# Optimization experiments

Hardware: AMD Instinct MI355X
Metric: run time of the kernel (lower is better)

## Reference

```python
import jax, jax.numpy as jnp
import numpy as np

N = 50000      # nodes
E = 800000     # edges (avg degree 16)
D_IN = 128
D_H = 128
D_OUT = 64
SLOPE = 0.2    # leaky-relu negative slope (from the 0.2 constants in the graph)


def setup_inputs() -> dict:
    key = jax.random.key(0)
    ks = jax.random.split(key, 18)
    def w(k, shape, fan_in):
        return jax.random.normal(k, shape, jnp.float32) / np.sqrt(fan_in)
    inp = {
        "x": jax.random.normal(ks[0], (N, D_IN), jnp.float32),
        "W0": w(ks[1], (D_IN, D_H), D_IN),
        "b0": jnp.zeros((D_H,), jnp.float32),
        "Wq1": w(ks[2], (D_H, D_H), D_H),
        "bq1": jnp.zeros((D_H,), jnp.float32),
        "Wp1": w(ks[3], (D_H, D_H), D_H),
        "bp1": jnp.zeros((D_H,), jnp.float32),
        "a1": 0.1 * w(ks[4], (D_H,), D_H),
        "bg2": jnp.zeros((D_H,), jnp.float32),
        "Wq2": w(ks[5], (D_H, D_OUT), D_H),
        "bq2": jnp.zeros((D_OUT,), jnp.float32),
        "Wp2": w(ks[6], (D_H, D_OUT), D_H),
        "bp2": jnp.zeros((D_OUT,), jnp.float32),
        "a2": 0.1 * w(ks[7], (D_OUT,), D_OUT),
        "b_out": jnp.zeros((D_OUT,), jnp.float32),
        "src": jax.random.randint(ks[8], (E,), 0, N),
        "dst": jax.random.randint(ks[9], (E,), 0, N),
        "num_nodes": N,
    }
    return inp


def _gat_block(m, src, dst, Wq, bq, Wp, bp, a, n):
    # m: [N, d_in]; q/p: [N, d]
    q = m @ Wq + bq
    p = m @ Wp + bp
    # edge scores: s_e = sum_d leaky_relu(q[dst_e] + p[src_e]) * a_d   [E]
    e = jax.nn.leaky_relu(q[dst] + p[src], SLOPE)          # [E, d]
    s = jnp.einsum("ed,d->e", e, a)                        # [E]
    es = jnp.exp(s)                                        # unstabilized exp, as in source graph
    denom = jax.ops.segment_sum(es, dst, num_segments=n)   # [N]
    alpha = es / denom[dst]                                # [E] edge softmax over incoming edges
    # aggregate messages alpha_e * p[src_e] into dst nodes
    agg = jax.ops.segment_sum(alpha[:, None] * p[src], dst, num_segments=n)  # [N, d]
    return agg


def reference(x, W0, b0, Wq1, bq1, Wp1, bp1, a1, bg2, Wq2, bq2, Wp2, bp2, a2, b_out, src, dst, num_nodes):
    m1 = jax.nn.gelu(x @ W0 + b0, approximate=False)       # erf GELU per graph constants
    h1 = _gat_block(m1, src, dst, Wq1, bq1, Wp1, bp1, a1, num_nodes)
    m2 = jax.nn.gelu(h1 + bg2, approximate=False)
    h2 = _gat_block(m2, src, dst, Wq2, bq2, Wp2, bp2, a2, num_nodes)
    return h2 + b_out
```

## Files before the change

### kernel.cpp

```cpp
#include <hip/hip_runtime.h>
#include <hip/hip_bf16.h>
#include <math.h>


#define SLOPE 0.2f

typedef __attribute__((ext_vector_type(8))) __bf16 bf16x8;
typedef __attribute__((ext_vector_type(4))) float f32x4;

__device__ __forceinline__ float gelu_erf(float x) {
    return 0.5f * x * (1.0f + erff(x * 0.70710678118654752f));
}

__device__ __forceinline__ unsigned short f2bf(float f) {
    unsigned int u = __float_as_uint(f);
    return (unsigned short)((u + 0x7fffu + ((u >> 16) & 1u)) >> 16);
}
__device__ __forceinline__ float bf2f(unsigned short h) {
    return __uint_as_float((unsigned int)h << 16);
}

__device__ __forceinline__ float row16_sum(float x) {
    x += __int_as_float(__builtin_amdgcn_update_dpp(0, __float_as_int(x), 0x121, 0xF, 0xF, true));
    x += __int_as_float(__builtin_amdgcn_update_dpp(0, __float_as_int(x), 0x122, 0xF, 0xF, true));
    x += __int_as_float(__builtin_amdgcn_update_dpp(0, __float_as_int(x), 0x124, 0xF, 0xF, true));
    x += __int_as_float(__builtin_amdgcn_update_dpp(0, __float_as_int(x), 0x128, 0xF, 0xF, true));
    return x;
}

__device__ __forceinline__ int swz(int off) { return off ^ ((off >> 4) & 0x70); }

__global__ __launch_bounds__(256) void pack_w(
    const float* __restrict__ W0,  const float* __restrict__ Wq1,
    const float* __restrict__ Wp1, const float* __restrict__ Wq2,
    const float* __restrict__ Wp2,
    unsigned short* __restrict__ P0,  unsigned short* __restrict__ Pq1,
    unsigned short* __restrict__ Pp1, unsigned short* __restrict__ Pq2,
    unsigned short* __restrict__ Pp2)
{
    const float* W; unsigned short* P; int C;
    switch (blockIdx.y) {
        case 0:  W = W0;  P = P0;  C = 128; break;
        case 1:  W = Wq1; P = Pq1; C = 128; break;
        case 2:  W = Wp1; P = Pp1; C = 128; break;
        case 3:  W = Wq2; P = Pq2; C = 64;  break;
        default: W = Wp2; P = Pp2; C = 64;  break;
    }
    int i = blockIdx.x * 256 + threadIdx.x;
    int CE = C * 128;
    if (i >= CE) return;
    int j = i & 7, l = (i >> 3) & 63, ks = (i >> 9) & 3, ct = i >> 11;
    int k = ks * 32 + ((l >> 4) << 3) + j;
    int n = ct * 16 + (l & 15);
    float v = W[k * C + n];
    unsigned short hb = f2bf(v);
    P[i] = hb;
    P[CE + i] = f2bf(v - bf2f(hb));
}

template <int C, bool TWO, int EPI>
__global__ __launch_bounds__(256) void mfma_gemm(
    const float* __restrict__ Af,
    const unsigned short* __restrict__ AHg, const unsigned short* __restrict__ ALg,
    const unsigned short* __restrict__ P1, const float* __restrict__ b1,
    const unsigned short* __restrict__ P2, const float* __restrict__ b2,
    float* __restrict__ outq, unsigned short* __restrict__ outp,
    unsigned short* __restrict__ o1hi, unsigned short* __restrict__ o1lo,
    int N)
{
    constexpr int CE  = C * 128;
    constexpr int CTT = (TWO ? 2 : 1) * (C / 16);
    constexpr int CTW = CTT / 4;
    constexpr int QCT = C / 16;

    __shared__ __align__(16) unsigned char lds[32768];

    const int t = threadIdx.x;
    const int lane = t & 63;
    const int w = t >> 6;
    const int row0 = blockIdx.x * 64;
    const int mcol = lane & 15;
    const int hk = lane >> 4;

    if constexpr (EPI == 0) {
#pragma unroll
        for (int i = 0; i < 8; i++) {
            int idx = t + i * 256;
            int row = idx >> 5;
            int gr = row0 + row;
            float4 v = make_float4(0.f, 0.f, 0.f, 0.f);
            if (gr < N) v = *reinterpret_cast<const float4*>(Af + (size_t)gr * 128 + (idx & 31) * 4);
            const float* f = reinterpret_cast<const float*>(&v);
            unsigned int h[4], l[4];
#pragma unroll
            for (int j = 0; j < 4; j++) {
                unsigned short hb = f2bf(f[j]);
                h[j] = hb;
                l[j] = f2bf(f[j] - bf2f(hb));
            }
            int so = swz(row * 256 + (idx & 31) * 8);
            *reinterpret_cast<uint2*>(&lds[so])         = make_uint2(h[0] | (h[1] << 16), h[2] | (h[3] << 16));
            *reinterpret_cast<uint2*>(&lds[16384 + so]) = make_uint2(l[0] | (l[1] << 16), l[2] | (l[3] << 16));
        }
    } else {
#pragma unroll
        for (int i = 0; i < 4; i++) {
            int idx = t + i * 256;
            int row = idx >> 4;
            int gr = row0 + row;
            uint4 vh = make_uint4(0, 0, 0, 0), vl = make_uint4(0, 0, 0, 0);
            if (gr < N) {
                vh = *reinterpret_cast<const uint4*>(AHg + (size_t)gr * 128 + (idx & 15) * 8);
                vl = *reinterpret_cast<const uint4*>(ALg + (size_t)gr * 128 + (idx & 15) * 8);
            }
            int so = swz(row * 256 + (idx & 15) * 16);
            *reinterpret_cast<uint4*>(&lds[so])         = vh;
            *reinterpret_cast<uint4*>(&lds[16384 + so]) = vl;
        }
    }
    __syncthreads();

    f32x4 acc[CTW][4];
#pragma unroll
    for (int c = 0; c < CTW; c++)
#pragma unroll
        for (int rf = 0; rf < 4; rf++) acc[c][rf] = (f32x4){0.f, 0.f, 0.f, 0.f};

#pragma unroll
    for (int ks = 0; ks < 4; ks++) {
        bf16x8 ah[4], al[4];
#pragma unroll
        for (int rf = 0; rf < 4; rf++) {
            int so = swz((rf * 16 + mcol) * 256 + ks * 64 + hk * 16);
            ah[rf] = *reinterpret_cast<const bf16x8*>(&lds[so]);
            al[rf] = *reinterpret_cast<const bf16x8*>(&lds[16384 + so]);
        }
#pragma unroll
        for (int c = 0; c < CTW; c++) {
            int ctg = w * CTW + c;
            bool isq = (!TWO) || (ctg < QCT);
            int ct = isq ? ctg : ctg - QCT;
            const unsigned short* P = isq ? P1 : P2;
            const unsigned short* Wp = P + ((ct * 4 + ks) * 64 + lane) * 8;
            bf16x8 bh = *reinterpret_cast<const bf16x8*>(Wp);
            bf16x8 bl = *reinterpret_cast<const bf16x8*>(Wp + CE);
#pragma unroll
            for (int rf = 0; rf < 4; rf++) {
                acc[c][rf] = __builtin_amdgcn_mfma_f32_16x16x32_bf16(ah[rf], bh, acc[c][rf], 0, 0, 0);
                acc[c][rf] = __builtin_amdgcn_mfma_f32_16x16x32_bf16(al[rf], bh, acc[c][rf], 0, 0, 0);
                acc[c][rf] = __builtin_amdgcn_mfma_f32_16x16x32_bf16(ah[rf], bl, acc[c][rf], 0, 0, 0);
            }
        }
    }

    __syncthreads();

    if constexpr (EPI == 0) {
#pragma unroll
        for (int c = 0; c < CTW; c++) {
            int col = (w * CTW + c) * 16 + mcol;
            float bv = b1[col];
#pragma unroll
            for (int rf = 0; rf < 4; rf++) {
#pragma unroll
                for (int r = 0; r < 4; r++) {
                    int row = rf * 16 + hk * 4 + r;
                    float v = gelu_erf(acc[c][rf][r] + bv);
                    unsigned short hb = f2bf(v);
                    int bo = row * 256 + col * 2;
                    *reinterpret_cast<unsigned short*>(&lds[swz(bo)])         = hb;
                    *reinterpret_cast<unsigned short*>(&lds[16384 + swz(bo)]) = f2bf(v - bf2f(hb));
                }
            }
        }
        __syncthreads();
#pragma unroll
        for (int i = 0; i < 8; i++) {
            int idx = t + i * 256;
            int pl = idx >> 10;
            int j = idx & 1023;
            int row = j >> 4;
            int gr = row0 + row;
            if (gr < N) {
                uint4 v = *reinterpret_cast<const uint4*>(&lds[pl * 16384 + swz(row * 256 + (j & 15) * 16)]);
                unsigned short* dp = pl ? o1lo : o1hi;
                *reinterpret_cast<uint4*>(dp + (size_t)gr * 128 + (j & 15) * 8) = v;
            }
        }
    } else {
#pragma unroll
        for (int c = 0; c < CTW; c++) {
            int ctg = w * CTW + c;
            bool isq = ctg < QCT;
            int ct = isq ? ctg : ctg - QCT;
            int col = ct * 16 + mcol;
            float bv = (isq ? b1 : b2)[col];
#pragma unroll
            for (int rf = 0; rf < 4; rf++) {
#pragma unroll
                for (int r = 0; r < 4; r++) {
                    int row = rf * 16 + hk * 4 + r;
                    int gr = row0 + row;
                    float v = acc[c][rf][r] + bv;
                    if (isq) {
                        if (gr < N) outq[(size_t)gr * C + col] = v;
                    } else {
                        *reinterpret_cast<unsigned short*>(&lds[swz(row * 256 + col * 2)]) = f2bf(v);
                    }
                }
            }
        }
        __syncthreads();
        constexpr int SLOTS = C / 8;
#pragma unroll
        for (int i = 0; i < (64 * SLOTS) / 256; i++) {
            int idx = t + i * 256;
            int row = idx / SLOTS;
            int sl = idx % SLOTS;
            int gr = row0 + row;
            if (gr < N)
                *reinterpret_cast<uint4*>(outp + (size_t)gr * C + sl * 8) =
                    *reinterpret_cast<const uint4*>(&lds[swz(row * 256 + sl * 16)]);
        }
    }
}


__global__ __launch_bounds__(256) void hist_coarse(
    const int* __restrict__ dst, int* __restrict__ gh, int E, int CB)
{
    __shared__ int cnt[4096];
    const int blk = blockIdx.x;
    const int t = threadIdx.x;
    for (int b = t; b < CB; b += 256) cnt[b] = 0;
    __syncthreads();
    const int epb = (E + 63) / 64;
    const int s = blk * epb;
    const int e_ = (s + epb < E) ? s + epb : E;
    for (int i = s + t; i < e_; i += 256)
        atomicAdd(&cnt[dst[i] >> 4], 1);
    __syncthreads();
    for (int b = t; b < CB; b += 256)
        gh[b * 64 + blk] = cnt[b];
}

__global__ __launch_bounds__(256) void scan1_kernel(const int* __restrict__ gh,
                                                    int* __restrict__ gscan,
                                                    int* __restrict__ bsum, int M)
{
    __shared__ int lds[256];
    int t = threadIdx.x;
    int i = blockIdx.x * 256 + t;
    int v = (i < M) ? gh[i] : 0;
    lds[t] = v;
    __syncthreads();
    int x = v;
    for (int off = 1; off < 256; off <<= 1) {
        int y = (t >= off) ? lds[t - off] : 0;
        __syncthreads();
        x += y;
        lds[t] = x;
        __syncthreads();
    }
    if (i < M) gscan[i] = x - v;
    if (t == 255) bsum[blockIdx.x] = x;
}

__global__ __launch_bounds__(1024) void scan2_kernel(int* __restrict__ bsum, int NB)
{
    __shared__ int lds[1024];
    int t = threadIdx.x;
    int v = (t < NB) ? bsum[t] : 0;
    lds[t] = v;
    __syncthreads();
    int x = v;
    for (int off = 1; off < 1024; off <<= 1) {
        int y = (t >= off) ? lds[t - off] : 0;
        __syncthreads();
        x += y;
        lds[t] = x;
        __syncthreads();
    }
    if (t < NB) bsum[t] = x - v;
}

__global__ __launch_bounds__(256) void scan3_kernel(int* __restrict__ gscan,
                                                    const int* __restrict__ bsum, int M)
{
    int i = blockIdx.x * 256 + threadIdx.x;
    if (i < M) gscan[i] += bsum[blockIdx.x];
}

__global__ __launch_bounds__(256) void scatter_coarse(
    const int* __restrict__ src, const int* __restrict__ dst,
    const int* __restrict__ gscan, int2* __restrict__ pairs, int E, int CB)
{
    __shared__ int cur[4096];
    const int blk = blockIdx.x;
    const int t = threadIdx.x;
    for (int b = t; b < CB; b += 256)
        cur[b] = gscan[b * 64 + blk];
    __syncthreads();
    const int epb = (E + 63) / 64;
    const int s = blk * epb;
    const int e_ = (s + epb < E) ? s + epb : E;
    for (int i = s + t; i < e_; i += 256) {
        int d = dst[i];
        int sv = src[i];
        int pos = atomicAdd(&cur[d >> 4], 1);
        pairs[pos] = make_int2(d, sv);
    }
}

__global__ __launch_bounds__(256) void finalize_kernel(
    const int2* __restrict__ pairs, const int* __restrict__ gscan,
    int* __restrict__ offs, int* __restrict__ csr_src, int N, int E, int CB)
{
    const int wid = blockIdx.x * 4 + (threadIdx.x >> 6);
    const int lane = threadIdx.x & 63;
    if (wid >= CB) return;

    const int s    = gscan[wid * 64];
    const int e_   = (wid + 1 < CB) ? gscan[(wid + 1) * 64] : E;
    const int base = wid * 16;
    const unsigned long long ltmask = (lane == 63) ? ~0ull >> 1
                                                   : (1ull << lane) - 1ull;

    int rc[16];
#pragma unroll
    for (int j = 0; j < 16; j++) rc[j] = 0;
    for (int c0 = s; c0 < e_; c0 += 64) {
        int i = c0 + lane;
        int d = (i < e_) ? pairs[i].x - base : -1;
#pragma unroll
        for (int j = 0; j < 16; j++)
            rc[j] += (int)__popcll(__ballot(d == j));
    }

    int pref[16];
    int run = s;
#pragma unroll
    for (int j = 0; j < 16; j++) { pref[j] = run; run += rc[j]; }
    int pref_v = 0;
#pragma unroll
    for (int j = 0; j < 16; j++) pref_v = (lane == j) ? pref[j] : pref_v;

    if (lane < 16 && base + lane < N) offs[base + lane] = pref_v;
    if (wid == CB - 1 && lane == 16) offs[N] = E;

    int rcv = 0;
    for (int c0 = s; c0 < e_; c0 += 64) {
        int i = c0 + lane;
        const bool act = i < e_;
        int2 pr = act ? pairs[i] : make_int2(base - 1, 0);
        int d = pr.x - base;
        unsigned long long msel = 0;
        int addcnt = 0;
#pragma unroll
        for (int j = 0; j < 16; j++) {
            unsigned long long m = __ballot(d == j);
            if (d == j) msel = m;
            if (lane == j) addcnt = (int)__popcll(m);
        }
        int subrank = (int)__popcll(msel & ltmask);
        int posbase = __builtin_amdgcn_ds_bpermute(d * 4, pref_v + rcv);
        if (act) csr_src[posbase + subrank] = pr.y;
        rcv += addcnt;
    }
}

template <int D, int EPI>
__global__ __launch_bounds__(256) void gat_agg(
    const float* __restrict__ q, const unsigned short* __restrict__ p,
    const float* __restrict__ a, const float* __restrict__ bvec,
    const int* __restrict__ offs, const int* __restrict__ csr_src,
    float* __restrict__ out, unsigned short* __restrict__ mhi,
    unsigned short* __restrict__ mlo, int N)
{
    constexpr int VPL = D / 16;
    const int t = threadIdx.x;
    const int lane = t & 63;
    const int sl = lane & 15;
    const int base = sl * VPL;
    const int node = blockIdx.x * 16 + ((t >> 6) << 2) + (lane >> 4);
    const bool valid = node < N;

    float qv[VPL], a6[VPL], a4[VPL], acc[VPL];
#pragma unroll
    for (int v = 0; v < VPL; v++) { qv[v] = 0.f; acc[v] = 0.f; }
    if (valid) {
        const float* qp = q + (size_t)node * D + base;
        float4 q0 = *reinterpret_cast<const float4*>(qp);
        qv[0] = q0.x; qv[1] = q0.y; qv[2] = q0.z; qv[3] = q0.w;
        if constexpr (VPL == 8) {
            float4 q1 = *reinterpret_cast<const float4*>(qp + 4);
            qv[4] = q1.x; qv[5] = q1.y; qv[6] = q1.z; qv[7] = q1.w;
        }
    }
#pragma unroll
    for (int v = 0; v < VPL; v++) {
        float av = a[base + v];
        a6[v] = 0.6f * av;
        a4[v] = 0.4f * av;
    }

    auto gather = [&](int s) -> uint4 {
        if constexpr (D == 128) {
            return *reinterpret_cast<const uint4*>(p + (size_t)s * 128 + base);
        } else {
            uint2 u = *reinterpret_cast<const uint2*>(p + (size_t)s * 64 + base);
            return make_uint4(u.x, u.y, 0u, 0u);
        }
    };
    auto unpack = [&](uint4 u, float* pv) {
        pv[0] = __uint_as_float(u.x << 16); pv[1] = __uint_as_float(u.x & 0xffff0000u);
        pv[2] = __uint_as_float(u.y << 16); pv[3] = __uint_as_float(u.y & 0xffff0000u);
        if constexpr (VPL == 8) {
            pv[4] = __uint_as_float(u.z << 16); pv[5] = __uint_as_float(u.z & 0xffff0000u);
            pv[6] = __uint_as_float(u.w << 16); pv[7] = __uint_as_float(u.w & 0xffff0000u);
        }
    };

    float denom = 0.f;
    int e  = valid ? offs[node] : 0;
    int e1 = valid ? offs[node + 1] : 0;

    int s0 = csr_src[(e + 0 < e1) ? e + 0 : 0];
    int s1 = csr_src[(e + 1 < e1) ? e + 1 : 0];
    int s2 = csr_src[(e + 2 < e1) ? e + 2 : 0];
    int s3 = csr_src[(e + 3 < e1) ? e + 3 : 0];
    uint4 uA0 = gather(s0), uA1 = gather(s1), uA2 = gather(s2), uA3 = gather(s3);
    int en = e + 4;
    int n0 = csr_src[(en + 0 < e1) ? en + 0 : 0];
    int n1 = csr_src[(en + 1 < e1) ? en + 1 : 0];
    int n2 = csr_src[(en + 2 < e1) ? en + 2 : 0];
    int n3 = csr_src[(en + 3 < e1) ? en + 3 : 0];

    while (__any(e < e1)) {
        const bool a0 = (e + 0) < e1, a1b = (e + 1) < e1,
                   a2 = (e + 2) < e1, a3 = (e + 3) < e1;

        uint4 v0 = gather(n0), v1 = gather(n1), v2 = gather(n2), v3 = gather(n3);

        const int em = en + 4;
        const int m0 = csr_src[(em + 0 < e1) ? em + 0 : 0];
        const int m1 = csr_src[(em + 1 < e1) ? em + 1 : 0];
        const int m2 = csr_src[(em + 2 < e1) ? em + 2 : 0];
        const int m3 = csr_src[(em + 3 < e1) ? em + 3 : 0];

        float pv[4][VPL];
        unpack(uA0, pv[0]); unpack(uA1, pv[1]); unpack(uA2, pv[2]); unpack(uA3, pv[3]);

        float pa0 = 0.f, pa1 = 0.f, pa2 = 0.f, pa3 = 0.f;
#pragma unroll
        for (int v = 0; v < VPL; v++) {
            float d0 = qv[v] + pv[0][v];
            float d1 = qv[v] + pv[1][v];
            float d2 = qv[v] + pv[2][v];
            float d3 = qv[v] + pv[3][v];
            pa0 = fmaf(d0, a6[v], pa0); pa0 = fmaf(fabsf(d0), a4[v], pa0);
            pa1 = fmaf(d1, a6[v], pa1); pa1 = fmaf(fabsf(d1), a4[v], pa1);
            pa2 = fmaf(d2, a6[v], pa2); pa2 = fmaf(fabsf(d2), a4[v], pa2);
            pa3 = fmaf(d3, a6[v], pa3); pa3 = fmaf(fabsf(d3), a4[v], pa3);
        }

        float r0 = row16_sum(pa0);
        float r1 = row16_sum(pa1);
        float r2 = row16_sum(pa2);
        float r3 = row16_sum(pa3);

        float esm0 = a0  ? __expf(r0) : 0.f;
        float esm1 = a1b ? __expf(r1) : 0.f;
        float esm2 = a2  ? __expf(r2) : 0.f;
        float esm3 = a3  ? __expf(r3) : 0.f;
        denom += (esm0 + esm1) + (esm2 + esm3);
#pragma unroll
        for (int v = 0; v < VPL; v++) {
            acc[v] = fmaf(esm0, pv[0][v], acc[v]);
            acc[v] = fmaf(esm1, pv[1][v], acc[v]);
            acc[v] = fmaf(esm2, pv[2][v], acc[v]);
            acc[v] = fmaf(esm3, pv[3][v], acc[v]);
        }

        uA0 = v0; uA1 = v1; uA2 = v2; uA3 = v3;
        n0 = m0; n1 = m1; n2 = m2; n3 = m3;
        e = en; en = em;
    }

    if (!valid) return;
    float inv = (denom != 0.f) ? 1.f / denom : 0.f;
    if constexpr (EPI == 0) {
        union { unsigned short us[8]; uint4 v; } H, L;
#pragma unroll
        for (int v = 0; v < VPL; v++) {
            float g = gelu_erf(acc[v] * inv + bvec[base + v]);
            H.us[v] = f2bf(g);
            L.us[v] = f2bf(g - bf2f(H.us[v]));
        }
        *reinterpret_cast<uint4*>(mhi + (size_t)node * 128 + base) = H.v;
        *reinterpret_cast<uint4*>(mlo + (size_t)node * 128 + base) = L.v;
    } else {
        union { float f[4]; float4 v; } O;
#pragma unroll
        for (int v = 0; v < VPL; v++) O.f[v] = acc[v] * inv + bvec[base + v];
        *reinterpret_cast<float4*>(out + (size_t)node * D + base) = O.v;
    }
}

extern "C" void kernel_launch(void* const* d_in, const int* in_sizes, int n_in,
                              void* d_out, int out_size, void* d_ws, size_t ws_size,
                              hipStream_t stream)
{
    const float* x     = (const float*)d_in[0];
    const float* W0    = (const float*)d_in[1];
    const float* b0    = (const float*)d_in[2];
    const float* Wq1   = (const float*)d_in[3];
    const float* bq1   = (const float*)d_in[4];
    const float* Wp1   = (const float*)d_in[5];
    const float* bp1   = (const float*)d_in[6];
    const float* a1    = (const float*)d_in[7];
    const float* bg2   = (const float*)d_in[8];
    const float* Wq2   = (const float*)d_in[9];
    const float* bq2   = (const float*)d_in[10];
    const float* Wp2   = (const float*)d_in[11];
    const float* bp2   = (const float*)d_in[12];
    const float* a2    = (const float*)d_in[13];
    const float* b_out = (const float*)d_in[14];
    const int*   src   = (const int*)d_in[15];
    const int*   dst   = (const int*)d_in[16];

    const int N = in_sizes[0] / 128;
    const int E = in_sizes[15];
    float* out = (float*)d_out;

    float* q_buf        = (float*)d_ws;
    unsigned short* pb  = (unsigned short*)(q_buf + (size_t)N * 128);
    unsigned short* Mhi = pb + (size_t)N * 128;
    unsigned short* Mlo = Mhi + (size_t)N * 128;
    unsigned short* P0  = Mlo + (size_t)N * 128;
    unsigned short* Pq1 = P0  + 128 * 128 * 2;
    unsigned short* Pp1 = Pq1 + 128 * 128 * 2;
    unsigned short* Pq2 = Pp1 + 128 * 128 * 2;
    unsigned short* Pp2 = Pq2 + 128 * 64 * 2;
    int* offs    = (int*)(Pp2 + 128 * 64 * 2);
    int* csr_src = offs + (N + 2);
    const int CB = (N + 15) / 16;
    const int M  = CB * 64;
    int* gh    = csr_src + E;
    int* gscan = gh + M;
    int* bsum  = gscan + M;
    int2* pairs = (int2*)q_buf;

    const int NB1 = (M + 255) / 256;

    pack_w<<<dim3(64, 5), 256, 0, stream>>>(W0, Wq1, Wp1, Wq2, Wp2,
                                            P0, Pq1, Pp1, Pq2, Pp2);
    hist_coarse<<<64, 256, 0, stream>>>(dst, gh, E, CB);
    scan1_kernel<<<NB1, 256, 0, stream>>>(gh, gscan, bsum, M);
    scan2_kernel<<<1, 1024, 0, stream>>>(bsum, NB1);
    scan3_kernel<<<NB1, 256, 0, stream>>>(gscan, bsum, M);
    scatter_coarse<<<64, 256, 0, stream>>>(src, dst, gscan, pairs, E, CB);
    finalize_kernel<<<(CB + 3) / 4, 256, 0, stream>>>(pairs, gscan, offs, csr_src, N, E, CB);

    const int GB64 = (N + 63) / 64;
    const int GGAT = (N + 15) / 16;

    mfma_gemm<128, false, 0><<<GB64, 256, 0, stream>>>(
        x, nullptr, nullptr, P0, b0, nullptr, nullptr,
        nullptr, nullptr, Mhi, Mlo, N);
    mfma_gemm<128, true, 1><<<GB64, 256, 0, stream>>>(
        nullptr, Mhi, Mlo, Pq1, bq1, Pp1, bp1,
        q_buf, pb, nullptr, nullptr, N);
    gat_agg<128, 0><<<GGAT, 256, 0, stream>>>(
        q_buf, pb, a1, bg2, offs, csr_src,
        nullptr, Mhi, Mlo, N);
    mfma_gemm<64, true, 1><<<GB64, 256, 0, stream>>>(
        nullptr, Mhi, Mlo, Pq2, bq2, Pp2, bp2,
        q_buf, pb, nullptr, nullptr, N);
    gat_agg<64, 1><<<GGAT, 256, 0, stream>>>(
        q_buf, pb, a2, b_out, offs, csr_src,
        out, nullptr, nullptr, N);
}
```

Measured before the change: 283.6 us.

## Fuse input GEMM with layer-1 projections and layer-1 aggregation with layer-2 GEMM

Merges the x@W0+GELU GEMM with the q/p projection GEMM for layer 1 so the GELU activations stay in LDS and never go to global memory. Also fuses the layer-1 attention aggregation with the layer-2 projection GEMM: each block aggregates 64 nodes in four passes, writes the GELU output into LDS as hi/lo bf16 and runs the MFMA GEMM directly. This removes two kernel launches and the global round trips of the M hi/lo buffers. The cost is fewer, larger blocks for the aggregation (64 rows per block instead of 16) and more register pressure.

```diff
diff --git a/kernel.cpp b/kernel.cpp
--- a/kernel.cpp
+++ b/kernel.cpp
@@ -58,21 +58,14 @@
     P[CE + i] = f2bf(v - bf2f(hb));
 }
 
-template <int C, bool TWO, int EPI>
-__global__ __launch_bounds__(256) void mfma_gemm(
-    const float* __restrict__ Af,
-    const unsigned short* __restrict__ AHg, const unsigned short* __restrict__ ALg,
-    const unsigned short* __restrict__ P1, const float* __restrict__ b1,
-    const unsigned short* __restrict__ P2, const float* __restrict__ b2,
-    float* __restrict__ outq, unsigned short* __restrict__ outp,
-    unsigned short* __restrict__ o1hi, unsigned short* __restrict__ o1lo,
-    int N)
-{
-    constexpr int CE  = C * 128;
-    constexpr int CTT = (TWO ? 2 : 1) * (C / 16);
-    constexpr int CTW = CTT / 4;
-    constexpr int QCT = C / 16;
-
+__global__ __launch_bounds__(256) void gemm_fused01(
+    const float* __restrict__ x,
+    const unsigned short* __restrict__ P0,  const float* __restrict__ b0,
+    const unsigned short* __restrict__ Pq1, const float* __restrict__ bq1,
+    const unsigned short* __restrict__ Pp1, const float* __restrict__ bp1,
+    float* __restrict__ outq, unsigned short* __restrict__ outp, int N)
+{
+    constexpr int CE = 128 * 128;
     __shared__ __align__(16) unsigned char lds[32768];
 
     const int t = threadIdx.x;
@@ -82,49 +75,32 @@
     const int mcol = lane & 15;
     const int hk = lane >> 4;
 
-    if constexpr (EPI == 0) {
-#pragma unroll
-        for (int i = 0; i < 8; i++) {
-            int idx = t + i * 256;
-            int row = idx >> 5;
-            int gr = row0 + row;
-            float4 v = make_float4(0.f, 0.f, 0.f, 0.f);
-            if (gr < N) v = *reinterpret_cast<const float4*>(Af + (size_t)gr * 128 + (idx & 31) * 4);
-            const float* f = reinterpret_cast<const float*>(&v);
-            unsigned int h[4], l[4];
-#pragma unroll
-            for (int j = 0; j < 4; j++) {
-                unsigned short hb = f2bf(f[j]);
-                h[j] = hb;
-                l[j] = f2bf(f[j] - bf2f(hb));
-            }
-            int so = swz(row * 256 + (idx & 31) * 8);
-            *reinterpret_cast<uint2*>(&lds[so])         = make_uint2(h[0] | (h[1] << 16), h[2] | (h[3] << 16));
-            *reinterpret_cast<uint2*>(&lds[16384 + so]) = make_uint2(l[0] | (l[1] << 16), l[2] | (l[3] << 16));
-        }
-    } else {
-#pragma unroll
-        for (int i = 0; i < 4; i++) {
-            int idx = t + i * 256;
-            int row = idx >> 4;
-            int gr = row0 + row;
-            uint4 vh = make_uint4(0, 0, 0, 0), vl = make_uint4(0, 0, 0, 0);
-            if (gr < N) {
-                vh = *reinterpret_cast<const uint4*>(AHg + (size_t)gr * 128 + (idx & 15) * 8);
-                vl = *reinterpret_cast<const uint4*>(ALg + (size_t)gr * 128 + (idx & 15) * 8);
-            }
-            int so = swz(row * 256 + (idx & 15) * 16);
-            *reinterpret_cast<uint4*>(&lds[so])         = vh;
-            *reinterpret_cast<uint4*>(&lds[16384 + so]) = vl;
-        }
-    }
-    __syncthreads();
-
-    f32x4 acc[CTW][4];
-#pragma unroll
-    for (int c = 0; c < CTW; c++)
-#pragma unroll
-        for (int rf = 0; rf < 4; rf++) acc[c][rf] = (f32x4){0.f, 0.f, 0.f, 0.f};
+#pragma unroll
+    for (int i = 0; i < 8; i++) {
+        int idx = t + i * 256;
+        int row = idx >> 5;
+        int gr = row0 + row;
+        float4 v = make_float4(0.f, 0.f, 0.f, 0.f);
+        if (gr < N) v = *reinterpret_cast<const float4*>(x + (size_t)gr * 128 + (idx & 31) * 4);
+        const float* f = reinterpret_cast<const float*>(&v);
+        unsigned int h[4], l[4];
+#pragma unroll
+        for (int j = 0; j < 4; j++) {
+            unsigned short hb = f2bf(f[j]);
+            h[j] = hb;
+            l[j] = f2bf(f[j] - bf2f(hb));
+        }
+        int so = swz(row * 256 + (idx & 31) * 8);
+        *reinterpret_cast<uint2*>(&lds[so])         = make_uint2(h[0] | (h[1] << 16), h[2] | (h[3] << 16));
+        *reinterpret_cast<uint2*>(&lds[16384 + so]) = make_uint2(l[0] | (l[1] << 16), l[2] | (l[3] << 16));
+    }
+    __syncthreads();
+
+    f32x4 acc1[2][4];
+#pragma unroll
+    for (int c = 0; c < 2; c++)
+#pragma unroll
+        for (int rf = 0; rf < 4; rf++) acc1[c][rf] = (f32x4){0.f, 0.f, 0.f, 0.f};
 
 #pragma unroll
     for (int ks = 0; ks < 4; ks++) {
@@ -136,92 +112,105 @@
             al[rf] = *reinterpret_cast<const bf16x8*>(&lds[16384 + so]);
         }
 #pragma unroll
-        for (int c = 0; c < CTW; c++) {
-            int ctg = w * CTW + c;
-            bool isq = (!TWO) || (ctg < QCT);
-            int ct = isq ? ctg : ctg - QCT;
-            const unsigned short* P = isq ? P1 : P2;
-            const unsigned short* Wp = P + ((ct * 4 + ks) * 64 + lane) * 8;
+        for (int c = 0; c < 2; c++) {
+            int ct = w * 2 + c;
+            const unsigned short* Wp = P0 + ((ct * 4 + ks) * 64 + lane) * 8;
             bf16x8 bh = *reinterpret_cast<const bf16x8*>(Wp);
             bf16x8 bl = *reinterpret_cast<const bf16x8*>(Wp + CE);
 #pragma unroll
             for (int rf = 0; rf < 4; rf++) {
-                acc[c][rf] = __builtin_amdgcn_mfma_f32_16x16x32_bf16(ah[rf], bh, acc[c][rf], 0, 0, 0);
-                acc[c][rf] = __builtin_amdgcn_mfma_f32_16x16x32_bf16(al[rf], bh, acc[c][rf], 0, 0, 0);
-                acc[c][rf] = __builtin_amdgcn_mfma_f32_16x16x32_bf16(ah[rf], bl, acc[c][rf], 0, 0, 0);
-            }
-        }
-    }
-
-    __syncthreads();
-
-    if constexpr (EPI == 0) {
-#pragma unroll
-        for (int c = 0; c < CTW; c++) {
-            int col = (w * CTW + c) * 16 + mcol;
-            float bv = b1[col];
+                acc1[c][rf] = __builtin_amdgcn_mfma_f32_16x16x32_bf16(ah[rf], bh, acc1[c][rf], 0, 0, 0);
+                acc1[c][rf] = __builtin_amdgcn_mfma_f32_16x16x32_bf16(al[rf], bh, acc1[c][rf], 0, 0, 0);
+                acc1[c][rf] = __builtin_amdgcn_mfma_f32_16x16x32_bf16(ah[rf], bl, acc1[c][rf], 0, 0, 0);
+            }
+        }
+    }
+    __syncthreads();
+
+#pragma unroll
+    for (int c = 0; c < 2; c++) {
+        int col = (w * 2 + c) * 16 + mcol;
+        float bv = b0[col];
+#pragma unroll
+        for (int rf = 0; rf < 4; rf++) {
+#pragma unroll
+            for (int r = 0; r < 4; r++) {
+                int row = rf * 16 + hk * 4 + r;
+                float v = gelu_erf(acc1[c][rf][r] + bv);
+                unsigned short hb = f2bf(v);
+                int bo = row * 256 + col * 2;
+                *reinterpret_cast<unsigned short*>(&lds[swz(bo)])         = hb;
+                *reinterpret_cast<unsigned short*>(&lds[16384 + swz(bo)]) = f2bf(v - bf2f(hb));
+            }
+        }
+    }
+    __syncthreads();
+
+    f32x4 acc2[4][4];
+#pragma unroll
+    for (int c = 0; c < 4; c++)
+#pragma unroll
+        for (int rf = 0; rf < 4; rf++) acc2[c][rf] = (f32x4){0.f, 0.f, 0.f, 0.f};
+
+#pragma unroll
+    for (int ks = 0; ks < 4; ks++) {
+        bf16x8 ah[4], al[4];
+#pragma unroll
+        for (int rf = 0; rf < 4; rf++) {
+            int so = swz((rf * 16 + mcol) * 256 + ks * 64 + hk * 16);
+            ah[rf] = *reinterpret_cast<const bf16x8*>(&lds[so]);
+            al[rf] = *reinterpret_cast<const bf16x8*>(&lds[16384 + so]);
+        }
+#pragma unroll
+        for (int c = 0; c < 4; c++) {
+            int ctg = w * 4 + c;
+            bool isq = ctg < 8;
+            int ct = isq ? ctg : ctg - 8;
+            const unsigned short* Wp = (isq ? Pq1 : Pp1) + ((ct * 4 + ks) * 64 + lane) * 8;
+            bf16x8 bh = *reinterpret_cast<const bf16x8*>(Wp);
+            bf16x8 bl = *reinterpret_cast<const bf16x8*>(Wp + CE);
 #pragma unroll
             for (int rf = 0; rf < 4; rf++) {
-#pragma unroll
-                for (int r = 0; r < 4; r++) {
-                    int row = rf * 16 + hk * 4 + r;
-                    float v = gelu_erf(acc[c][rf][r] + bv);
-                    unsigned short hb = f2bf(v);
-                    int bo = row * 256 + col * 2;
-                    *reinterpret_cast<unsigned short*>(&lds[swz(bo)])         = hb;
-                    *reinterpret_cast<unsigned short*>(&lds[16384 + swz(bo)]) = f2bf(v - bf2f(hb));
+                acc2[c][rf] = __builtin_amdgcn_mfma_f32_16x16x32_bf16(ah[rf], bh, acc2[c][rf], 0, 0, 0);
+                acc2[c][rf] = __builtin_amdgcn_mfma_f32_16x16x32_bf16(al[rf], bh, acc2[c][rf], 0, 0, 0);
+                acc2[c][rf] = __builtin_amdgcn_mfma_f32_16x16x32_bf16(ah[rf], bl, acc2[c][rf], 0, 0, 0);
+            }
+        }
+    }
+    __syncthreads();
+
+#pragma unroll
+    for (int c = 0; c < 4; c++) {
+        int ctg = w * 4 + c;
+        bool isq = ctg < 8;
+        int ct = isq ? ctg : ctg - 8;
+        int col = ct * 16 + mcol;
+        float bv = (isq ? bq1 : bp1)[col];
+#pragma unroll
+        for (int rf = 0; rf < 4; rf++) {
+#pragma unroll
+            for (int r = 0; r < 4; r++) {
+                int row = rf * 16 + hk * 4 + r;
+                int gr = row0 + row;
+                float v = acc2[c][rf][r] + bv;
+                if (isq) {
+                    if (gr < N) outq[(size_t)gr * 128 + col] = v;
+                } else {
+                    *reinterpret_cast<unsigned short*>(&lds[swz(row * 256 + col * 2)]) = f2bf(v);
                 }
             }
         }
-        __syncthreads();
-#pragma unroll
-        for (int i = 0; i < 8; i++) {
-            int idx = t + i * 256;
-            int pl = idx >> 10;
-            int j = idx & 1023;
-            int row = j >> 4;
-            int gr = row0 + row;
-            if (gr < N) {
-                uint4 v = *reinterpret_cast<const uint4*>(&lds[pl * 16384 + swz(row * 256 + (j & 15) * 16)]);
-                unsigned short* dp = pl ? o1lo : o1hi;
-                *reinterpret_cast<uint4*>(dp + (size_t)gr * 128 + (j & 15) * 8) = v;
-            }
-        }
-    } else {
-#pragma unroll
-        for (int c = 0; c < CTW; c++) {
-            int ctg = w * CTW + c;
-            bool isq = ctg < QCT;
-            int ct = isq ? ctg : ctg - QCT;
-            int col = ct * 16 + mcol;
-            float bv = (isq ? b1 : b2)[col];
-#pragma unroll
-            for (int rf = 0; rf < 4; rf++) {
-#pragma unroll
-                for (int r = 0; r < 4; r++) {
-                    int row = rf * 16 + hk * 4 + r;
-                    int gr = row0 + row;
-                    float v = acc[c][rf][r] + bv;
-                    if (isq) {
-                        if (gr < N) outq[(size_t)gr * C + col] = v;
-                    } else {
-                        *reinterpret_cast<unsigned short*>(&lds[swz(row * 256 + col * 2)]) = f2bf(v);
-                    }
-                }
-            }
-        }
-        __syncthreads();
-        constexpr int SLOTS = C / 8;
-#pragma unroll
-        for (int i = 0; i < (64 * SLOTS) / 256; i++) {
-            int idx = t + i * 256;
-            int row = idx / SLOTS;
-            int sl = idx % SLOTS;
-            int gr = row0 + row;
-            if (gr < N)
-                *reinterpret_cast<uint4*>(outp + (size_t)gr * C + sl * 8) =
-                    *reinterpret_cast<const uint4*>(&lds[swz(row * 256 + sl * 16)]);
-        }
+    }
+    __syncthreads();
+#pragma unroll
+    for (int i = 0; i < 4; i++) {
+        int idx = t + i * 256;
+        int row = idx >> 4;
+        int sl = idx & 15;
+        int gr = row0 + row;
+        if (gr < N)
+            *reinterpret_cast<uint4*>(outp + (size_t)gr * 128 + sl * 8) =
+                *reinterpret_cast<const uint4*>(&lds[swz(row * 256 + sl * 16)]);
     }
 }
 
@@ -369,56 +358,245 @@
     }
 }
 
-template <int D, int EPI>
-__global__ __launch_bounds__(256) void gat_agg(
+__global__ __launch_bounds__(256) void gat_gemm2(
     const float* __restrict__ q, const unsigned short* __restrict__ p,
-    const float* __restrict__ a, const float* __restrict__ bvec,
+    const float* __restrict__ a, const float* __restrict__ bg2,
     const int* __restrict__ offs, const int* __restrict__ csr_src,
-    float* __restrict__ out, unsigned short* __restrict__ mhi,
-    unsigned short* __restrict__ mlo, int N)
-{
-    constexpr int VPL = D / 16;
+    const unsigned short* __restrict__ Pq2, const float* __restrict__ bq2,
+    const unsigned short* __restrict__ Pp2, const float* __restrict__ bp2,
+    float* __restrict__ outq2, unsigned short* __restrict__ outp2, int N)
+{
+    constexpr int CE = 64 * 128;
+    __shared__ __align__(16) unsigned char lds[32768];
+
     const int t = threadIdx.x;
     const int lane = t & 63;
+    const int w = t >> 6;
     const int sl = lane & 15;
-    const int base = sl * VPL;
-    const int node = blockIdx.x * 16 + ((t >> 6) << 2) + (lane >> 4);
-    const bool valid = node < N;
-
-    float qv[VPL], a6[VPL], a4[VPL], acc[VPL];
-#pragma unroll
-    for (int v = 0; v < VPL; v++) { qv[v] = 0.f; acc[v] = 0.f; }
-    if (valid) {
-        const float* qp = q + (size_t)node * D + base;
-        float4 q0 = *reinterpret_cast<const float4*>(qp);
-        qv[0] = q0.x; qv[1] = q0.y; qv[2] = q0.z; qv[3] = q0.w;
-        if constexpr (VPL == 8) {
-            float4 q1 = *reinterpret_cast<const float4*>(qp + 4);
-            qv[4] = q1.x; qv[5] = q1.y; qv[6] = q1.z; qv[7] = q1.w;
-        }
-    }
-#pragma unroll
-    for (int v = 0; v < VPL; v++) {
+    const int base = sl * 8;
+    const int row0 = blockIdx.x * 64;
+
+    float a6[8], a4[8];
+#pragma unroll
+    for (int v = 0; v < 8; v++) {
         float av = a[base + v];
         a6[v] = 0.6f * av;
         a4[v] = 0.4f * av;
     }
 
     auto gather = [&](int s) -> uint4 {
-        if constexpr (D == 128) {
-            return *reinterpret_cast<const uint4*>(p + (size_t)s * 128 + base);
-        } else {
-            uint2 u = *reinterpret_cast<const uint2*>(p + (size_t)s * 64 + base);
-            return make_uint4(u.x, u.y, 0u, 0u);
-        }
+        return *reinterpret_cast<const uint4*>(p + (size_t)s * 128 + base);
     };
     auto unpack = [&](uint4 u, float* pv) {
         pv[0] = __uint_as_float(u.x << 16); pv[1] = __uint_as_float(u.x & 0xffff0000u);
         pv[2] = __uint_as_float(u.y << 16); pv[3] = __uint_as_float(u.y & 0xffff0000u);
-        if constexpr (VPL == 8) {
-            pv[4] = __uint_as_float(u.z << 16); pv[5] = __uint_as_float(u.z & 0xffff0000u);
-            pv[6] = __uint_as_float(u.w << 16); pv[7] = __uint_as_float(u.w & 0xffff0000u);
-        }
+        pv[4] = __uint_as_float(u.z << 16); pv[5] = __uint_as_float(u.z & 0xffff0000u);
+        pv[6] = __uint_as_float(u.w << 16); pv[7] = __uint_as_float(u.w & 0xffff0000u);
+    };
+
+    for (int pass = 0; pass < 4; pass++) {
+        const int row = pass * 16 + w * 4 + (lane >> 4);
+        const int node = row0 + row;
+        const bool valid = node < N;
+
+        float qv[8], acc[8];
+#pragma unroll
+        for (int v = 0; v < 8; v++) { qv[v] = 0.f; acc[v] = 0.f; }
+        if (valid) {
+            const float* qp = q + (size_t)node * 128 + base;
+            float4 q0 = *reinterpret_cast<const float4*>(qp);
+            float4 q1 = *reinterpret_cast<const float4*>(qp + 4);
+            qv[0] = q0.x; qv[1] = q0.y; qv[2] = q0.z; qv[3] = q0.w;
+            qv[4] = q1.x; qv[5] = q1.y; qv[6] = q1.z; qv[7] = q1.w;
+        }
+
+        float denom = 0.f;
+        int e  = valid ? offs[node] : 0;
+        int e1 = valid ? offs[node + 1] : 0;
+
+        int s0 = csr_src[(e + 0 < e1) ? e + 0 : 0];
+        int s1 = csr_src[(e + 1 < e1) ? e + 1 : 0];
+        int s2 = csr_src[(e + 2 < e1) ? e + 2 : 0];
+        int s3 = csr_src[(e + 3 < e1) ? e + 3 : 0];
+        uint4 uA0 = gather(s0), uA1 = gather(s1), uA2 = gather(s2), uA3 = gather(s3);
+        int en = e + 4;
+        int n0 = csr_src[(en + 0 < e1) ? en + 0 : 0];
+        int n1 = csr_src[(en + 1 < e1) ? en + 1 : 0];
+        int n2 = csr_src[(en + 2 < e1) ? en + 2 : 0];
+        int n3 = csr_src[(en + 3 < e1) ? en + 3 : 0];
+
+        while (__any(e < e1)) {
+            const bool a0 = (e + 0) < e1, a1b = (e + 1) < e1,
+                       a2 = (e + 2) < e1, a3 = (e + 3) < e1;
+
+            uint4 v0 = gather(n0), v1 = gather(n1), v2 = gather(n2), v3 = gather(n3);
+
+            const int em = en + 4;
+            const int m0 = csr_src[(em + 0 < e1) ? em + 0 : 0];
+            const int m1 = csr_src[(em + 1 < e1) ? em + 1 : 0];
+            const int m2 = csr_src[(em + 2 < e1) ? em + 2 : 0];
+            const int m3 = csr_src[(em + 3 < e1) ? em + 3 : 0];
+
+            float pv[4][8];
+            unpack(uA0, pv[0]); unpack(uA1, pv[1]); unpack(uA2, pv[2]); unpack(uA3, pv[3]);
+
+            float pa0 = 0.f, pa1 = 0.f, pa2 = 0.f, pa3 = 0.f;
+#pragma unroll
+            for (int v = 0; v < 8; v++) {
+                float d0 = qv[v] + pv[0][v];
+                float d1 = qv[v] + pv[1][v];
+                float d2 = qv[v] + pv[2][v];
+                float d3 = qv[v] + pv[3][v];
+                pa0 = fmaf(d0, a6[v], pa0); pa0 = fmaf(fabsf(d0), a4[v], pa0);
+                pa1 = fmaf(d1, a6[v], pa1); pa1 = fmaf(fabsf(d1), a4[v], pa1);
+                pa2 = fmaf(d2, a6[v], pa2); pa2 = fmaf(fabsf(d2), a4[v], pa2);
+                pa3 = fmaf(d3, a6[v], pa3); pa3 = fmaf(fabsf(d3), a4[v], pa3);
+            }
+
+            float r0 = row16_sum(pa0);
+            float r1 = row16_sum(pa1);
+            float r2 = row16_sum(pa2);
+            float r3 = row16_sum(pa3);
+
+            float esm0 = a0  ? __expf(r0) : 0.f;
+            float esm1 = a1b ? __expf(r1) : 0.f;
+            float esm2 = a2  ? __expf(r2) : 0.f;
+            float esm3 = a3  ? __expf(r3) : 0.f;
+            denom += (esm0 + esm1) + (esm2 + esm3);
+#pragma unroll
+            for (int v = 0; v < 8; v++) {
+                acc[v] = fmaf(esm0, pv[0][v], acc[v]);
+                acc[v] = fmaf(esm1, pv[1][v], acc[v]);
+                acc[v] = fmaf(esm2, pv[2][v], acc[v]);
+                acc[v] = fmaf(esm3, pv[3][v], acc[v]);
+            }
+
+            uA0 = v0; uA1 = v1; uA2 = v2; uA3 = v3;
+            n0 = m0; n1 = m1; n2 = m2; n3 = m3;
+            e = en; en = em;
+        }
+
+        float inv = (denom != 0.f) ? 1.f / denom : 0.f;
+        union { unsigned short us[8]; uint4 v; } H, L;
+#pragma unroll
+        for (int v = 0; v < 8; v++) {
+            if (valid) {
+                float g = gelu_erf(acc[v] * inv + bg2[base + v]);
+                H.us[v] = f2bf(g);
+                L.us[v] = f2bf(g - bf2f(H.us[v]));
+            } else {
+                H.us[v] = 0; L.us[v] = 0;
+            }
+        }
+        int so = swz(row * 256 + sl * 16);
+        *reinterpret_cast<uint4*>(&lds[so])         = H.v;
+        *reinterpret_cast<uint4*>(&lds[16384 + so]) = L.v;
+    }
+    __syncthreads();
+
+    const int mcol = sl;
+    const int hk = lane >> 4;
+    f32x4 acc2[2][4];
+#pragma unroll
+    for (int c = 0; c < 2; c++)
+#pragma unroll
+        for (int rf = 0; rf < 4; rf++) acc2[c][rf] = (f32x4){0.f, 0.f, 0.f, 0.f};
+
+#pragma unroll
+    for (int ks = 0; ks < 4; ks++) {
+        bf16x8 ah[4], al[4];
+#pragma unroll
+        for (int rf = 0; rf < 4; rf++) {
+            int so = swz((rf * 16 + mcol) * 256 + ks * 64 + hk * 16);
+            ah[rf] = *reinterpret_cast<const bf16x8*>(&lds[so]);
+            al[rf] = *reinterpret_cast<const bf16x8*>(&lds[16384 + so]);
+        }
+#pragma unroll
+        for (int c = 0; c < 2; c++) {
+            int ctg = w * 2 + c;
+            bool isq = ctg < 4;
+            int ct = isq ? ctg : ctg - 4;
+            const unsigned short* Wp = (isq ? Pq2 : Pp2) + ((ct * 4 + ks) * 64 + lane) * 8;
+            bf16x8 bh = *reinterpret_cast<const bf16x8*>(Wp);
+            bf16x8 bl = *reinterpret_cast<const bf16x8*>(Wp + CE);
+#pragma unroll
+            for (int rf = 0; rf < 4; rf++) {
+                acc2[c][rf] = __builtin_amdgcn_mfma_f32_16x16x32_bf16(ah[rf], bh, acc2[c][rf], 0, 0, 0);
+                acc2[c][rf] = __builtin_amdgcn_mfma_f32_16x16x32_bf16(al[rf], bh, acc2[c][rf], 0, 0, 0);
+                acc2[c][rf] = __builtin_amdgcn_mfma_f32_16x16x32_bf16(ah[rf], bl, acc2[c][rf], 0, 0, 0);
+            }
+        }
+    }
+    __syncthreads();
+
+#pragma unroll
+    for (int c = 0; c < 2; c++) {
+        int ctg = w * 2 + c;
+        bool isq = ctg < 4;
+        int ct = isq ? ctg : ctg - 4;
+        int col = ct * 16 + mcol;
+        float bv = (isq ? bq2 : bp2)[col];
+#pragma unroll
+        for (int rf = 0; rf < 4; rf++) {
+#pragma unroll
+            for (int r = 0; r < 4; r++) {
+                int row = rf * 16 + hk * 4 + r;
+                int gr = row0 + row;
+                float v = acc2[c][rf][r] + bv;
+                if (isq) {
+                    if (gr < N) outq2[(size_t)gr * 64 + col] = v;
+                } else {
+                    *reinterpret_cast<unsigned short*>(&lds[swz(row * 256 + col * 2)]) = f2bf(v);
+                }
+            }
+        }
+    }
+    __syncthreads();
+#pragma unroll
+    for (int i = 0; i < 2; i++) {
+        int idx = t + i * 256;
+        int row = idx >> 3;
+        int sl8 = idx & 7;
+        int gr = row0 + row;
+        if (gr < N)
+            *reinterpret_cast<uint4*>(outp2 + (size_t)gr * 64 + sl8 * 8) =
+                *reinterpret_cast<const uint4*>(&lds[swz(row * 256 + sl8 * 16)]);
+    }
+}
+
+__global__ __launch_bounds__(256) void gat_agg64(
+    const float* __restrict__ q, const unsigned short* __restrict__ p,
+    const float* __restrict__ a, const float* __restrict__ bvec,
+    const int* __restrict__ offs, const int* __restrict__ csr_src,
+    float* __restrict__ out, int N)
+{
+    const int t = threadIdx.x;
+    const int lane = t & 63;
+    const int sl = lane & 15;
+    const int base = sl * 4;
+    const int node = blockIdx.x * 16 + ((t >> 6) << 2) + (lane >> 4);
+    const bool valid = node < N;
+
+    float qv[4], a6[4], a4[4], acc[4];
+#pragma unroll
+    for (int v = 0; v < 4; v++) { qv[v] = 0.f; acc[v] = 0.f; }
+    if (valid) {
+        float4 q0 = *reinterpret_cast<const float4*>(q + (size_t)node * 64 + base);
+        qv[0] = q0.x; qv[1] = q0.y; qv[2] = q0.z; qv[3] = q0.w;
+    }
+#pragma unroll
+    for (int v = 0; v < 4; v++) {
+        float av = a[base + v];
+        a6[v] = 0.6f * av;
+        a4[v] = 0.4f * av;
+    }
+
+    auto gather = [&](int s) -> uint2 {
+        return *reinterpret_cast<const uint2*>(p + (size_t)s * 64 + base);
+    };
+    auto unpack = [&](uint2 u, float* pv) {
+        pv[0] = __uint_as_float(u.x << 16); pv[1] = __uint_as_float(u.x & 0xffff0000u);
+        pv[2] = __uint_as_float(u.y << 16); pv[3] = __uint_as_float(u.y & 0xffff0000u);
     };
 
     float denom = 0.f;
@@ -429,7 +607,7 @@
     int s1 = csr_src[(e + 1 < e1) ? e + 1 : 0];
     int s2 = csr_src[(e + 2 < e1) ? e + 2 : 0];
     int s3 = csr_src[(e + 3 < e1) ? e + 3 : 0];
-    uint4 uA0 = gather(s0), uA1 = gather(s1), uA2 = gather(s2), uA3 = gather(s3);
+    uint2 uA0 = gather(s0), uA1 = gather(s1), uA2 = gather(s2), uA3 = gather(s3);
     int en = e + 4;
     int n0 = csr_src[(en + 0 < e1) ? en + 0 : 0];
     int n1 = csr_src[(en + 1 < e1) ? en + 1 : 0];
@@ -440,7 +618,7 @@
         const bool a0 = (e + 0) < e1, a1b = (e + 1) < e1,
                    a2 = (e + 2) < e1, a3 = (e + 3) < e1;
 
-        uint4 v0 = gather(n0), v1 = gather(n1), v2 = gather(n2), v3 = gather(n3);
+        uint2 v0 = gather(n0), v1 = gather(n1), v2 = gather(n2), v3 = gather(n3);
 
         const int em = en + 4;
         const int m0 = csr_src[(em + 0 < e1) ? em + 0 : 0];
@@ -448,12 +626,12 @@
         const int m2 = csr_src[(em + 2 < e1) ? em + 2 : 0];
         const int m3 = csr_src[(em + 3 < e1) ? em + 3 : 0];
 
-        float pv[4][VPL];
+        float pv[4][4];
         unpack(uA0, pv[0]); unpack(uA1, pv[1]); unpack(uA2, pv[2]); unpack(uA3, pv[3]);
 
         float pa0 = 0.f, pa1 = 0.f, pa2 = 0.f, pa3 = 0.f;
 #pragma unroll
-        for (int v = 0; v < VPL; v++) {
+        for (int v = 0; v < 4; v++) {
             float d0 = qv[v] + pv[0][v];
             float d1 = qv[v] + pv[1][v];
             float d2 = qv[v] + pv[2][v];
@@ -475,7 +653,7 @@
         float esm3 = a3  ? __expf(r3) : 0.f;
         denom += (esm0 + esm1) + (esm2 + esm3);
 #pragma unroll
-        for (int v = 0; v < VPL; v++) {
+        for (int v = 0; v < 4; v++) {
             acc[v] = fmaf(esm0, pv[0][v], acc[v]);
             acc[v] = fmaf(esm1, pv[1][v], acc[v]);
             acc[v] = fmaf(esm2, pv[2][v], acc[v]);
@@ -489,22 +667,10 @@
 
     if (!valid) return;
     float inv = (denom != 0.f) ? 1.f / denom : 0.f;
-    if constexpr (EPI == 0) {
-        union { unsigned short us[8]; uint4 v; } H, L;
-#pragma unroll
-        for (int v = 0; v < VPL; v++) {
-            float g = gelu_erf(acc[v] * inv + bvec[base + v]);
-            H.us[v] = f2bf(g);
-            L.us[v] = f2bf(g - bf2f(H.us[v]));
-        }
-        *reinterpret_cast<uint4*>(mhi + (size_t)node * 128 + base) = H.v;
-        *reinterpret_cast<uint4*>(mlo + (size_t)node * 128 + base) = L.v;
-    } else {
-        union { float f[4]; float4 v; } O;
-#pragma unroll
-        for (int v = 0; v < VPL; v++) O.f[v] = acc[v] * inv + bvec[base + v];
-        *reinterpret_cast<float4*>(out + (size_t)node * D + base) = O.v;
-    }
+    union { float f[4]; float4 v; } O;
+#pragma unroll
+    for (int v = 0; v < 4; v++) O.f[v] = acc[v] * inv + bvec[base + v];
+    *reinterpret_cast<float4*>(out + (size_t)node * 64 + base) = O.v;
 }
 
 extern "C" void kernel_launch(void* const* d_in, const int* in_sizes, int n_in,
@@ -550,6 +716,8 @@
     int* gscan = gh + M;
     int* bsum  = gscan + M;
     int2* pairs = (int2*)q_buf;
+    float* q2f = (float*)Mhi;
+    unsigned short* p2b = Mlo;
 
     const int NB1 = (M + 255) / 256;
 
@@ -563,21 +731,12 @@
     finalize_kernel<<<(CB + 3) / 4, 256, 0, stream>>>(pairs, gscan, offs, csr_src, N, E, CB);
 
     const int GB64 = (N + 63) / 64;
-    const int GGAT = (N + 15) / 16;
-
-    mfma_gemm<128, false, 0><<<GB64, 256, 0, stream>>>(
-        x, nullptr, nullptr, P0, b0, nullptr, nullptr,
-        nullptr, nullptr, Mhi, Mlo, N);
-    mfma_gemm<128, true, 1><<<GB64, 256, 0, stream>>>(
-        nullptr, Mhi, Mlo, Pq1, bq1, Pp1, bp1,
-        q_buf, pb, nullptr, nullptr, N);
-    gat_agg<128, 0><<<GGAT, 256, 0, stream>>>(
+
+    gemm_fused01<<<GB64, 256, 0, stream>>>(
+        x, P0, b0, Pq1, bq1, Pp1, bp1, q_buf, pb, N);
+    gat_gemm2<<<GB64, 256, 0, stream>>>(
         q_buf, pb, a1, bg2, offs, csr_src,
-        nullptr, Mhi, Mlo, N);
-    mfma_gemm<64, true, 1><<<GB64, 256, 0, stream>>>(
-        nullptr, Mhi, Mlo, Pq2, bq2, Pp2, bp2,
-        q_buf, pb, nullptr, nullptr, N);
-    gat_agg<64, 1><<<GGAT, 256, 0, stream>>>(
-        q_buf, pb, a2, b_out, offs, csr_src,
-        out, nullptr, nullptr, N);
-}
+        Pq2, bq2, Pp2, bp2, q2f, p2b, N);
+    gat_agg64<<<(N + 15) / 16, 256, 0, stream>>>(
+        q2f, p2b, a2, b_out, offs, csr_src, out, N);
+}
```

New measurement: 302.6 us. 6.7% more time.
